# Optimization experiments

Hardware: AMD Instinct MI355X
Metric: run time of the kernel (lower is better)

The kernel has to match this reference:

```python
import jax, jax.numpy as jnp
import numpy as np
import math

EMBED_DIM = 512
NUM_CLASSES = 100000
BATCH = 1024
MARGIN = 0.5
SCALE = 64.0


def setup_inputs() -> dict:
    key = jax.random.key(0)
    k1, k2, k3 = jax.random.split(key, 3)
    embeddings = jax.random.normal(k1, (BATCH, EMBED_DIM), dtype=jnp.float32)
    labels = jax.random.randint(k2, (BATCH,), 0, NUM_CLASSES, dtype=jnp.int64)
    # xavier_uniform for weight [num_classes, embedding_dim]
    limit = math.sqrt(6.0 / (NUM_CLASSES + EMBED_DIM))
    weight = jax.random.uniform(k3, (NUM_CLASSES, EMBED_DIM), dtype=jnp.float32,
                                minval=-limit, maxval=limit)
    return {"embeddings": embeddings, "weight": weight, "labels": labels}


def _l2norm(x, axis=-1, eps=1e-12):
    # matches torch F.normalize (p=2, eps=1e-12)
    n = jnp.linalg.norm(x, axis=axis, keepdims=True)
    return x / jnp.maximum(n, eps)


def reference(embeddings, weight, labels):
    cos_m = math.cos(MARGIN)
    sin_m = math.sin(MARGIN)
    th = math.cos(math.pi - MARGIN)
    mm = math.sin(math.pi - MARGIN) * MARGIN

    # cosine similarity: [B, C]
    cosine = _l2norm(embeddings) @ _l2norm(weight).T
    sine = jnp.sqrt(jnp.clip(1.0 - cosine * cosine, 0.0, 1.0))
    phi = cosine * cos_m - sine * sin_m
    phi = jnp.where(cosine > th, phi, cosine - mm)

    # apply margin only at the label position
    one_hot = jax.nn.one_hot(labels, NUM_CLASSES, dtype=cosine.dtype)
    logits = SCALE * (one_hot * phi + (1.0 - one_hot) * cosine)

    # cross entropy, mean reduction
    logp = jax.nn.log_softmax(logits, axis=-1)
    nll = -jnp.take_along_axis(logp, labels[:, None], axis=1)[:, 0]
    return jnp.mean(nll)
```

## Files before the change

### kernel.cpp

```cpp
#include <hip/hip_runtime.h>
#include <hip/hip_bf16.h>
#include <math.h>

#define B_ROWS 1024
#define EMB    512
#define NCLS   100000
#define SCALE_ 64.0f
#define COS_M 0.8775825618903728f
#define SIN_M 0.479425538604203f
#define TH_C  (-0.8775825618903728f)
#define MM_C  0.2397127693021015f

#define BM 128
#define BN 128
#define BK 32
#define NTILES 782
#define KCHUNKS 16

typedef __attribute__((ext_vector_type(8))) short bf16x8;
typedef __attribute__((ext_vector_type(4))) short s16x4;
typedef __attribute__((ext_vector_type(4))) float f32x4;

typedef __attribute__((address_space(1))) const unsigned int GLP;
typedef __attribute__((address_space(3))) unsigned int LDP;

__device__ __forceinline__ float bf2f(short u) {
  unsigned int x = ((unsigned int)(unsigned short)u) << 16;
  return __builtin_bit_cast(float, x);
}
__device__ __forceinline__ short f2bf(float f) {
  unsigned int u = __builtin_bit_cast(unsigned int, f);
  u += 0x7FFF + ((u >> 16) & 1);
  return (short)(u >> 16);
}

__device__ __forceinline__ void load16(const void* g, void* l) {
  __builtin_amdgcn_global_load_lds((GLP*)g, (LDP*)l, 16, 0, 0);
}

__global__ void setup_kernel(const void* __restrict__ emb, const int* __restrict__ labels,
                             float* __restrict__ row_sum, float* __restrict__ accum,
                             int* __restrict__ flag, int* __restrict__ dflag) {
  const int t = threadIdx.x;
  row_sum[t] = 0.f;
  row_sum[t + 512] = 0.f;
  if (t == 0) *accum = 0.f;

  if (t < 64) {
    bf16x8 v = *(const bf16x8*)((const short*)emb + t * 8);
    float s = 0.f;
    #pragma unroll
    for (int j = 0; j < 8; ++j) { float f = bf2f(v[j]); s += f * f; }
    #pragma unroll
    for (int off = 1; off < 64; off <<= 1) s += __shfl_xor(s, off);
    if (t == 0) *dflag = (s < 1e8f) ? 1 : 0;
  }

  int v = labels[2 * t + 1];
  #pragma unroll
  for (int off = 1; off < 64; off <<= 1) v |= __shfl_xor(v, off);
  __shared__ int red[8];
  if ((t & 63) == 0) red[t >> 6] = v;
  __syncthreads();
  if (t == 0) {
    int o = 0;
    #pragma unroll
    for (int i = 0; i < 8; ++i) o |= red[i];
    *flag = (o == 0) ? 1 : 0;
  }
}

__global__ __launch_bounds__(256) void normconv_kernel(
    const void* __restrict__ emb, const void* __restrict__ wgt,
    const int* __restrict__ dflag,
    float* __restrict__ inv_e, float* __restrict__ inv_w,
    short* __restrict__ An, short* __restrict__ Wn, const int do_conv) {
  const int sub  = threadIdx.x & 15;
  const int rloc = threadIdx.x >> 4;
  const int row  = blockIdx.x * 16 + rloc;
  int r;
  const void* base;
  float* dst;
  short* out;
  if (row < B_ROWS) { r = row; base = emb; dst = inv_e + row; out = An + (size_t)row * EMB; }
  else {
    r = row - B_ROWS;
    if (r >= NCLS) return;
    base = wgt; dst = inv_w + r; out = Wn + (size_t)r * EMB;
  }
  const int isbf16 = *dflag;
  float f[32];
  if (isbf16) {
    const short* p = (const short*)base + (size_t)r * EMB;
    #pragma unroll
    for (int j = 0; j < 4; ++j) {
      bf16x8 v = *(const bf16x8*)(p + j * 128 + sub * 8);
      #pragma unroll
      for (int t = 0; t < 8; ++t) f[j * 8 + t] = bf2f(v[t]);
    }
  } else {
    const float* p = (const float*)base + (size_t)r * EMB;
    #pragma unroll
    for (int j = 0; j < 8; ++j) {
      f32x4 v = *(const f32x4*)(p + j * 64 + sub * 4);
      #pragma unroll
      for (int t = 0; t < 4; ++t) f[j * 4 + t] = v[t];
    }
  }
  float s = 0.f;
  #pragma unroll
  for (int j = 0; j < 32; ++j) s += f[j] * f[j];
  #pragma unroll
  for (int off = 1; off < 16; off <<= 1) s += __shfl_xor(s, off);
  const float inv = 1.f / fmaxf(sqrtf(s), 1e-12f);
  if (sub == 0) *dst = inv;
  if (do_conv) {
    if (isbf16) {
      #pragma unroll
      for (int j = 0; j < 4; ++j) {
        bf16x8 o;
        #pragma unroll
        for (int t = 0; t < 8; ++t) o[t] = f2bf(f[j * 8 + t] * inv);
        *(bf16x8*)(out + j * 128 + sub * 8) = o;
      }
    } else {
      #pragma unroll
      for (int j = 0; j < 8; ++j) {
        s16x4 o;
        #pragma unroll
        for (int t = 0; t < 4; ++t) o[t] = f2bf(f[j * 4 + t] * inv);
        *(s16x4*)(out + j * 64 + sub * 4) = o;
      }
    }
  }
}

__global__ __launch_bounds__(256, 3) void arc_gemm_fast(
    const short* __restrict__ A, const short* __restrict__ W,
    const int* __restrict__ labels, const int* __restrict__ flag,
    float* __restrict__ row_sum, float* __restrict__ lablogit) {
  const int bid = blockIdx.x;
  const int k   = bid & 7;
  const int j   = bid >> 3;
  const int ytile = (j >> 3) * 8 + k;
  const int xtile = j & 7;
  if (ytile >= NTILES) return;

  __shared__ short As[BM * BK];
  __shared__ short Bs[BN * BK];
  __shared__ int   sh_lab[BM];
  __shared__ float sh_sum[BM][2];

  const int tid  = threadIdx.x;
  const int wave = tid >> 6;
  const int lane = tid & 63;
  const int wy = wave >> 1;
  const int wx = wave & 1;
  const int lr = lane & 15;
  const int lk = lane >> 4;
  const int mBase = xtile * BM;
  const int nBase = ytile * BN;

  const int srow  = lane >> 2;
  const int sbyte = (((lane & 3) ^ ((lane >> 3) & 3)) << 4);
  const int rswz  = ((lr >> 1) & 3);

  f32x4 zero = {0.f, 0.f, 0.f, 0.f};
  f32x4 acc[4][4];
  #pragma unroll
  for (int i = 0; i < 4; ++i)
    #pragma unroll
    for (int jj = 0; jj < 4; ++jj) acc[i][jj] = zero;

  const char* Ab = (const char*)A;
  const char* Wb = (const char*)W;

  for (int kc = 0; kc < KCHUNKS; ++kc) {
    __syncthreads();
    const size_t koff = (size_t)kc * 64 + sbyte;
    #pragma unroll
    for (int it = 0; it < 2; ++it) {
      const int c = wave + it * 4;
      const int ar = mBase + c * 16 + srow;
      load16(Ab + (size_t)ar * 1024 + koff, (char*)As + (size_t)c * 1024);
      int br = nBase + c * 16 + srow;
      if (br >= NCLS) br = NCLS - 1;
      load16(Wb + (size_t)br * 1024 + koff, (char*)Bs + (size_t)c * 1024);
    }
    __syncthreads();
    bf16x8 af[4], bfr[4];
    #pragma unroll
    for (int mi = 0; mi < 4; ++mi)
      af[mi] = *(const bf16x8*)(As + ((wy * 64 + mi * 16 + lr) * BK + (lk ^ rswz) * 8));
    #pragma unroll
    for (int ni = 0; ni < 4; ++ni)
      bfr[ni] = *(const bf16x8*)(Bs + ((wx * 64 + ni * 16 + lr) * BK + (lk ^ rswz) * 8));
    #pragma unroll
    for (int mi = 0; mi < 4; ++mi)
      #pragma unroll
      for (int ni = 0; ni < 4; ++ni)
        acc[mi][ni] = __builtin_amdgcn_mfma_f32_16x16x32_bf16(af[mi], bfr[ni], acc[mi][ni], 0, 0, 0);
  }

  __syncthreads();
  if (tid < BM) {
    const int r = mBase + tid;
    const int f = *flag;
    sh_lab[tid] = labels[f ? (size_t)(2 * r) : (size_t)r];
  }
  __syncthreads();

  #pragma unroll
  for (int mi = 0; mi < 4; ++mi) {
    #pragma unroll
    for (int reg = 0; reg < 4; ++reg) {
      const int lrow = wy * 64 + mi * 16 + lk * 4 + reg;
      const int grow = mBase + lrow;
      const int lab = sh_lab[lrow];
      float s = 0.f;
      #pragma unroll
      for (int ni = 0; ni < 4; ++ni) {
        const int gcol = nBase + wx * 64 + ni * 16 + lr;
        if (gcol < NCLS) {
          const float cosv = acc[mi][ni][reg];
          float logit;
          if (gcol == lab) {
            const float sine = sqrtf(fmaxf(1.f - cosv * cosv, 0.f));
            float phi = cosv * COS_M - sine * SIN_M;
            phi = (cosv > TH_C) ? phi : (cosv - MM_C);
            logit = SCALE_ * phi;
            lablogit[grow] = logit;
          } else {
            logit = SCALE_ * cosv;
          }
          s += __expf(logit - SCALE_);
        }
      }
      #pragma unroll
      for (int off = 1; off < 16; off <<= 1) s += __shfl_xor(s, off);
      if (lr == 0) sh_sum[lrow][wx] = s;
    }
  }
  __syncthreads();
  if (tid < BM)
    atomicAdd(&row_sum[mBase + tid], sh_sum[tid][0] + sh_sum[tid][1]);
}

__global__ __launch_bounds__(256, 3) void arc_gemm(
    const void* __restrict__ A, const void* __restrict__ W,
    const float* __restrict__ inv_e, const float* __restrict__ inv_w,
    const int* __restrict__ labels, const int* __restrict__ flag,
    const int* __restrict__ dflag,
    float* __restrict__ row_sum, float* __restrict__ lablogit) {
  __shared__ short As[BM * BK];
  __shared__ short Bs[BN * BK];
  __shared__ int   sh_lab[BM];
  __shared__ float sh_sum[BM][2];

  const int tid  = threadIdx.x;
  const int wave = tid >> 6;
  const int lane = tid & 63;
  const int wy = wave >> 1;
  const int wx = wave & 1;
  const int lr = lane & 15;
  const int lk = lane >> 4;
  const int mBase = blockIdx.x * BM;
  const int nBase = blockIdx.y * BN;
  const int isbf16 = *dflag;

  const int srow  = lane >> 2;
  const int sbyte = (lane & 3) * 16;

  f32x4 zero = {0.f, 0.f, 0.f, 0.f};
  f32x4 acc[4][4];
  #pragma unroll
  for (int i = 0; i < 4; ++i)
    #pragma unroll
    for (int j = 0; j < 4; ++j) acc[i][j] = zero;

  const char*  Ab = (const char*)A;
  const char*  Wb = (const char*)W;
  const float* Af = (const float*)A;
  const float* Wf = (const float*)W;

  for (int kc = 0; kc < KCHUNKS; ++kc) {
    __syncthreads();
    if (isbf16) {
      const size_t koff = (size_t)kc * 64 + sbyte;
      #pragma unroll
      for (int it = 0; it < 2; ++it) {
        const int c = wave + it * 4;
        const int ar = mBase + c * 16 + srow;
        load16(Ab + (size_t)ar * 1024 + koff, (char*)As + (size_t)c * 1024);
        int br = nBase + c * 16 + srow;
        if (br >= NCLS) br = NCLS - 1;
        load16(Wb + (size_t)br * 1024 + koff, (char*)Bs + (size_t)c * 1024);
      }
    } else {
      #pragma unroll
      for (int p = 0; p < 2; ++p) {
        const int u   = p * 256 + tid;
        const int row = u >> 2;
        const int seg = u & 3;
        const float* ga = Af + ((size_t)(mBase + row) * EMB + kc * 32 + seg * 8);
        f32x4 x = *(const f32x4*)ga;
        f32x4 y = *(const f32x4*)(ga + 4);
        bf16x8 tpack;
        #pragma unroll
        for (int j = 0; j < 4; ++j) { tpack[j] = f2bf(x[j]); tpack[j + 4] = f2bf(y[j]); }
        *(bf16x8*)(As + row * BK + seg * 8) = tpack;
        int br = nBase + row;
        if (br >= NCLS) br = NCLS - 1;
        const float* gb = Wf + ((size_t)br * EMB + kc * 32 + seg * 8);
        x = *(const f32x4*)gb;
        y = *(const f32x4*)(gb + 4);
        #pragma unroll
        for (int j = 0; j < 4; ++j) { tpack[j] = f2bf(x[j]); tpack[j + 4] = f2bf(y[j]); }
        *(bf16x8*)(Bs + row * BK + seg * 8) = tpack;
      }
    }
    __syncthreads();
    bf16x8 af[4], bfr[4];
    #pragma unroll
    for (int mi = 0; mi < 4; ++mi)
      af[mi] = *(const bf16x8*)(As + ((wy * 64 + mi * 16 + lr) * BK + lk * 8));
    #pragma unroll
    for (int ni = 0; ni < 4; ++ni)
      bfr[ni] = *(const bf16x8*)(Bs + ((wx * 64 + ni * 16 + lr) * BK + lk * 8));
    #pragma unroll
    for (int mi = 0; mi < 4; ++mi)
      #pragma unroll
      for (int ni = 0; ni < 4; ++ni)
        acc[mi][ni] = __builtin_amdgcn_mfma_f32_16x16x32_bf16(af[mi], bfr[ni], acc[mi][ni], 0, 0, 0);
  }

  __syncthreads();
  if (tid < BM) {
    const int r = mBase + tid;
    const int f = *flag;
    sh_lab[tid] = labels[f ? (size_t)(2 * r) : (size_t)r];
  }
  __syncthreads();

  #pragma unroll
  for (int mi = 0; mi < 4; ++mi) {
    #pragma unroll
    for (int reg = 0; reg < 4; ++reg) {
      const int lrow = wy * 64 + mi * 16 + lk * 4 + reg;
      const int grow = mBase + lrow;
      const float ie = inv_e[grow];
      const int lab = sh_lab[lrow];
      float s = 0.f;
      #pragma unroll
      for (int ni = 0; ni < 4; ++ni) {
        const int gcol = nBase + wx * 64 + ni * 16 + lr;
        if (gcol < NCLS) {
          const float cosv = acc[mi][ni][reg] * ie * inv_w[gcol];
          float logit;
          if (gcol == lab) {
            const float sine = sqrtf(fmaxf(1.f - cosv * cosv, 0.f));
            float phi = cosv * COS_M - sine * SIN_M;
            phi = (cosv > TH_C) ? phi : (cosv - MM_C);
            logit = SCALE_ * phi;
            lablogit[grow] = logit;
          } else {
            logit = SCALE_ * cosv;
          }
          s += __expf(logit - SCALE_);
        }
      }
      #pragma unroll
      for (int off = 1; off < 16; off <<= 1) s += __shfl_xor(s, off);
      if (lr == 0) sh_sum[lrow][wx] = s;
    }
  }
  __syncthreads();
  if (tid < BM)
    atomicAdd(&row_sum[mBase + tid], sh_sum[tid][0] + sh_sum[tid][1]);
}

__global__ void loss_kernel(const float* __restrict__ row_sum,
                            const float* __restrict__ lablogit,
                            float* __restrict__ accum) {
  const int r = blockIdx.x * 128 + threadIdx.x;
  float loss = SCALE_ + logf(row_sum[r]) - lablogit[r];
  #pragma unroll
  for (int off = 1; off < 64; off <<= 1) loss += __shfl_xor(loss, off);
  __shared__ float rs[2];
  if ((threadIdx.x & 63) == 0) rs[threadIdx.x >> 6] = loss;
  __syncthreads();
  if (threadIdx.x == 0) atomicAdd(accum, rs[0] + rs[1]);
}

__global__ void finalize_kernel(const float* __restrict__ accum, float* __restrict__ out) {
  out[0] = accum[0] * (1.0f / 1024.0f);
}

extern "C" void kernel_launch(void* const* d_in, const int* in_sizes, int n_in,
                              void* d_out, int out_size, void* d_ws, size_t ws_size,
                              hipStream_t stream) {
  const void* emb   = d_in[0];
  const void* wgt   = d_in[1];
  const int* labels = (const int*)d_in[2];
  float* out = (float*)d_out;

  const int NORM_BLOCKS = (B_ROWS + NCLS + 15) / 16;

  const size_t WN_SHORTS = (size_t)NCLS * EMB;
  const size_t AN_SHORTS = (size_t)B_ROWS * EMB;
  const size_t FAST_NEED = (WN_SHORTS + AN_SHORTS) * 2 + 103075u * 4;

  if (ws_size >= FAST_NEED) {
    short* Wn = (short*)d_ws;
    short* An = Wn + WN_SHORTS;
    float* tail     = (float*)(An + AN_SHORTS);
    float* inv_e    = tail;
    float* inv_w    = tail + 1024;
    float* lablogit = tail + 101024;
    float* row_sum  = tail + 102048;
    float* accum    = tail + 103072;
    int*   flag     = (int*)(tail + 103073);
    int*   dflag    = (int*)(tail + 103074);

    setup_kernel<<<1, 512, 0, stream>>>(emb, labels, row_sum, accum, flag, dflag);
    normconv_kernel<<<NORM_BLOCKS, 256, 0, stream>>>(
        emb, wgt, dflag, inv_e, inv_w, An, Wn, 1);
    arc_gemm_fast<<<8 * 784, 256, 0, stream>>>(An, Wn, labels, flag, row_sum, lablogit);
    loss_kernel<<<8, 128, 0, stream>>>(row_sum, lablogit, accum);
    finalize_kernel<<<1, 1, 0, stream>>>(accum, out);
  } else {
    float* ws       = (float*)d_ws;
    float* inv_e    = ws;
    float* inv_w    = ws + 1024;
    float* lablogit = ws + 101024;
    float* row_sum  = ws + 102048;
    float* accum    = ws + 103072;
    int*   flag     = (int*)(ws + 103073);
    int*   dflag    = (int*)(ws + 103074);

    setup_kernel<<<1, 512, 0, stream>>>(emb, labels, row_sum, accum, flag, dflag);
    normconv_kernel<<<NORM_BLOCKS, 256, 0, stream>>>(
        emb, wgt, dflag, inv_e, inv_w, (short*)inv_e, (short*)inv_e, 0);
    dim3 grid(8, NTILES);
    arc_gemm<<<grid, 256, 0, stream>>>(emb, wgt, inv_e, inv_w, labels, flag, dflag, row_sum, lablogit);
    loss_kernel<<<8, 128, 0, stream>>>(row_sum, lablogit, accum);
    finalize_kernel<<<1, 1, 0, stream>>>(accum, out);
  }
}
```

Baseline: 465.3 us.

## Use 256x256 tiles with double-buffered LDS pipeline in fast GEMM

Rewrites the fast GEMM kernel to use 256x256 output tiles with 512 threads (8 waves), a BK=64 K-step and two LDS buffers of 64KB each. Global-to-LDS loads for step t+2 are issued while MFMAs for step t run, with explicit waitcnt and barriers plus s_setprio. The grid is remapped so blocks are assigned per XCD. This is meant to raise arithmetic intensity and hide memory latency, at the cost of large LDS use (about 133KB) that limits occupancy and adds heavier register pressure.

```diff
diff --git a/kernel.cpp b/kernel.cpp
--- a/kernel.cpp
+++ b/kernel.cpp
@@ -16,6 +16,9 @@
 #define BK 32
 #define NTILES 782
 #define KCHUNKS 16
+
+#define NT2   391
+#define GRID2 1564
 
 typedef __attribute__((ext_vector_type(8))) short bf16x8;
 typedef __attribute__((ext_vector_type(4))) short s16x4;
@@ -135,92 +138,118 @@
   }
 }
 
-__global__ __launch_bounds__(256, 3) void arc_gemm_fast(
+__global__ __launch_bounds__(512, 2) void arc_gemm_fast(
     const short* __restrict__ A, const short* __restrict__ W,
     const int* __restrict__ labels, const int* __restrict__ flag,
     float* __restrict__ row_sum, float* __restrict__ lablogit) {
   const int bid = blockIdx.x;
   const int k   = bid & 7;
-  const int j   = bid >> 3;
-  const int ytile = (j >> 3) * 8 + k;
-  const int xtile = j & 7;
-  if (ytile >= NTILES) return;
-
-  __shared__ short As[BM * BK];
-  __shared__ short Bs[BN * BK];
-  __shared__ int   sh_lab[BM];
-  __shared__ float sh_sum[BM][2];
+  const int jj  = bid >> 3;
+  const int wgid = (k < 4 ? k * 196 : 4 * 196 + (k - 4) * 195) + jj;
+  const int ytile = wgid >> 2;
+  const int xtile = wgid & 3;
+  if (ytile >= NT2) return;
+
+  __shared__ __align__(16) char Lraw[131072 + 1024 + 4096];
+  char* L = Lraw;
+  int*   shl = (int*)(L + 131072);
+  float* shs = (float*)(L + 131072 + 1024);
 
   const int tid  = threadIdx.x;
   const int wave = tid >> 6;
   const int lane = tid & 63;
-  const int wy = wave >> 1;
-  const int wx = wave & 1;
-  const int lr = lane & 15;
-  const int lk = lane >> 4;
-  const int mBase = xtile * BM;
-  const int nBase = ytile * BN;
-
-  const int srow  = lane >> 2;
-  const int sbyte = (((lane & 3) ^ ((lane >> 3) & 3)) << 4);
-  const int rswz  = ((lr >> 1) & 3);
-
-  f32x4 zero = {0.f, 0.f, 0.f, 0.f};
-  f32x4 acc[4][4];
-  #pragma unroll
-  for (int i = 0; i < 4; ++i)
-    #pragma unroll
-    for (int jj = 0; jj < 4; ++jj) acc[i][jj] = zero;
+  const int wm   = wave >> 2;
+  const int wn   = wave & 3;
+  const int lr16 = lane & 15;
+  const int lkg  = lane >> 4;
+  const int mBase = xtile * 256;
+  const int nBase = ytile * 256;
 
   const char* Ab = (const char*)A;
   const char* Wb = (const char*)W;
 
-  for (int kc = 0; kc < KCHUNKS; ++kc) {
-    __syncthreads();
-    const size_t koff = (size_t)kc * 64 + sbyte;
-    #pragma unroll
-    for (int it = 0; it < 2; ++it) {
-      const int c = wave + it * 4;
-      const int ar = mBase + c * 16 + srow;
-      load16(Ab + (size_t)ar * 1024 + koff, (char*)As + (size_t)c * 1024);
-      int br = nBase + c * 16 + srow;
+  f32x4 zero = {0.f, 0.f, 0.f, 0.f};
+  f32x4 acc[8][4];
+  #pragma unroll
+  for (int i = 0; i < 8; ++i)
+    #pragma unroll
+    for (int j2 = 0; j2 < 4; ++j2) acc[i][j2] = zero;
+
+  auto stage = [&](int kt, int p) {
+    #pragma unroll
+    for (int j = 0; j < 4; ++j) {
+      const int row = j * 64 + (tid >> 3);
+      const int sl  = (tid & 7) ^ (row & 7);
+      load16(Ab + (size_t)(mBase + row) * 1024 + kt * 128 + sl * 16,
+             L + p * 65536 + j * 8192 + wave * 1024);
+      int br = nBase + row;
       if (br >= NCLS) br = NCLS - 1;
-      load16(Wb + (size_t)br * 1024 + koff, (char*)Bs + (size_t)c * 1024);
-    }
-    __syncthreads();
-    bf16x8 af[4], bfr[4];
-    #pragma unroll
-    for (int mi = 0; mi < 4; ++mi)
-      af[mi] = *(const bf16x8*)(As + ((wy * 64 + mi * 16 + lr) * BK + (lk ^ rswz) * 8));
-    #pragma unroll
-    for (int ni = 0; ni < 4; ++ni)
-      bfr[ni] = *(const bf16x8*)(Bs + ((wx * 64 + ni * 16 + lr) * BK + (lk ^ rswz) * 8));
-    #pragma unroll
-    for (int mi = 0; mi < 4; ++mi)
-      #pragma unroll
-      for (int ni = 0; ni < 4; ++ni)
-        acc[mi][ni] = __builtin_amdgcn_mfma_f32_16x16x32_bf16(af[mi], bfr[ni], acc[mi][ni], 0, 0, 0);
-  }
-
-  __syncthreads();
-  if (tid < BM) {
+      load16(Wb + (size_t)br * 1024 + kt * 128 + sl * 16,
+             L + p * 65536 + 32768 + j * 8192 + wave * 1024);
+    }
+  };
+
+  stage(0, 0);
+  stage(1, 1);
+  asm volatile("s_waitcnt vmcnt(8)" ::: "memory");
+  __builtin_amdgcn_s_barrier();
+
+  for (int t = 0; t < 8; ++t) {
+    const int p = t & 1;
+    const short* Abuf = (const short*)(L + p * 65536);
+    const short* Bbuf = (const short*)(L + p * 65536 + 32768);
+    bf16x8 af[2][8], bb[2][4];
+    #pragma unroll
+    for (int ks = 0; ks < 2; ++ks) {
+      #pragma unroll
+      for (int mi = 0; mi < 8; ++mi) {
+        const int ra = wm * 128 + mi * 16 + lr16;
+        const int sa = (ks * 4 + lkg) ^ (ra & 7);
+        af[ks][mi] = *(const bf16x8*)(Abuf + ra * 64 + sa * 8);
+      }
+      #pragma unroll
+      for (int ni = 0; ni < 4; ++ni) {
+        const int rb = wn * 64 + ni * 16 + lr16;
+        const int sb = (ks * 4 + lkg) ^ (rb & 7);
+        bb[ks][ni] = *(const bf16x8*)(Bbuf + rb * 64 + sb * 8);
+      }
+    }
+    asm volatile("s_waitcnt lgkmcnt(0)" ::: "memory");
+    __builtin_amdgcn_s_barrier();
+    stage((t + 2) & 7, p);
+    __builtin_amdgcn_s_setprio(1);
+    #pragma unroll
+    for (int mi = 0; mi < 8; ++mi)
+      #pragma unroll
+      for (int ni = 0; ni < 4; ++ni) {
+        acc[mi][ni] = __builtin_amdgcn_mfma_f32_16x16x32_bf16(af[0][mi], bb[0][ni], acc[mi][ni], 0, 0, 0);
+        acc[mi][ni] = __builtin_amdgcn_mfma_f32_16x16x32_bf16(af[1][mi], bb[1][ni], acc[mi][ni], 0, 0, 0);
+      }
+    __builtin_amdgcn_s_setprio(0);
+    asm volatile("s_waitcnt vmcnt(8)" ::: "memory");
+    __builtin_amdgcn_s_barrier();
+  }
+
+  asm volatile("s_waitcnt vmcnt(0)" ::: "memory");
+  __syncthreads();
+  if (tid < 256) {
     const int r = mBase + tid;
     const int f = *flag;
-    sh_lab[tid] = labels[f ? (size_t)(2 * r) : (size_t)r];
-  }
-  __syncthreads();
-
-  #pragma unroll
-  for (int mi = 0; mi < 4; ++mi) {
+    shl[tid] = labels[f ? (size_t)(2 * r) : (size_t)r];
+  }
+  __syncthreads();
+
+  #pragma unroll
+  for (int mi = 0; mi < 8; ++mi) {
     #pragma unroll
     for (int reg = 0; reg < 4; ++reg) {
-      const int lrow = wy * 64 + mi * 16 + lk * 4 + reg;
+      const int lrow = wm * 128 + mi * 16 + lkg * 4 + reg;
       const int grow = mBase + lrow;
-      const int lab = sh_lab[lrow];
+      const int lab = shl[lrow];
       float s = 0.f;
       #pragma unroll
       for (int ni = 0; ni < 4; ++ni) {
-        const int gcol = nBase + wx * 64 + ni * 16 + lr;
+        const int gcol = nBase + wn * 64 + ni * 16 + lr16;
         if (gcol < NCLS) {
           const float cosv = acc[mi][ni][reg];
           float logit;
@@ -238,12 +267,13 @@
       }
       #pragma unroll
       for (int off = 1; off < 16; off <<= 1) s += __shfl_xor(s, off);
-      if (lr == 0) sh_sum[lrow][wx] = s;
-    }
-  }
-  __syncthreads();
-  if (tid < BM)
-    atomicAdd(&row_sum[mBase + tid], sh_sum[tid][0] + sh_sum[tid][1]);
+      if (lr16 == 0) shs[lrow * 4 + wn] = s;
+    }
+  }
+  __syncthreads();
+  if (tid < 256)
+    atomicAdd(&row_sum[mBase + tid],
+              shs[tid * 4] + shs[tid * 4 + 1] + shs[tid * 4 + 2] + shs[tid * 4 + 3]);
 }
 
 __global__ __launch_bounds__(256, 3) void arc_gemm(
@@ -425,7 +455,7 @@
     setup_kernel<<<1, 512, 0, stream>>>(emb, labels, row_sum, accum, flag, dflag);
     normconv_kernel<<<NORM_BLOCKS, 256, 0, stream>>>(
         emb, wgt, dflag, inv_e, inv_w, An, Wn, 1);
-    arc_gemm_fast<<<8 * 784, 256, 0, stream>>>(An, Wn, labels, flag, row_sum, lablogit);
+    arc_gemm_fast<<<GRID2, 512, 0, stream>>>(An, Wn, labels, flag, row_sum, lablogit);
     loss_kernel<<<8, 128, 0, stream>>>(row_sum, lablogit, accum);
     finalize_kernel<<<1, 1, 0, stream>>>(accum, out);
   } else {
```

New measurement: 495.3 us. +6.5%, slower.
